# Optimization experiments

Measured on AMD Instinct MI355X. Metric: run time of the kernel, lower is better.

Reference implementation:

```python
import jax, jax.numpy as jnp
import numpy as np

T, B, E, H = 2048, 2, 1024, 16
DH = E // H  # head_dim = 64


def setup_inputs() -> dict:
    key = jax.random.key(0)
    ks = jax.random.split(key, 5)
    query = jax.random.normal(ks[0], (T, B, E), dtype=jnp.float32)
    # self-attention: key/value are passed but unused by the module
    k_in = query
    v_in = query
    # xavier-ish scaled params
    in_proj_weight = jax.random.normal(ks[1], (3 * E, E), dtype=jnp.float32) * (E ** -0.5)
    in_proj_bias = jnp.zeros((3 * E,), dtype=jnp.float32)
    out_w = jax.random.normal(ks[2], (E, E), dtype=jnp.float32) * (E ** -0.5)
    out_b = jnp.zeros((E,), dtype=jnp.float32)
    return {"query": query, "key": k_in, "value": v_in,
            "in_proj_weight": in_proj_weight, "in_proj_bias": in_proj_bias,
            "out_w": out_w, "out_b": out_b}


def reference(query, key, value, in_proj_weight, in_proj_bias, out_w, out_b):
    # query: [T, B, E] (fairseq Time x Batch x Channel)
    t, b, e = query.shape
    scaling = DH ** -0.5
    # fused QKV projection: in_proj_weight [3E, E]
    qkv = jnp.einsum('tbe,fe->tbf', query, in_proj_weight) + in_proj_bias  # [T,B,3E]
    q, k, v = jnp.split(qkv, 3, axis=-1)
    q = q * scaling
    # split heads -> [T, B, H, DH]
    q = q.reshape(t, b, H, DH)
    k = k.reshape(t, b, H, DH)
    v = v.reshape(t, b, H, DH)
    # attention scores [B, H, T, T]
    scores = jnp.einsum('tbhd,sbhd->bhts', q, k)
    probs = jax.nn.softmax(scores, axis=-1)
    # weighted sum -> [T, B, H, DH] -> [T, B, E]
    attn = jnp.einsum('bhts,sbhd->tbhd', probs, v).reshape(t, b, e)
    # output projection (LinearSuper with sample dims == super dims)
    out = jnp.einsum('tbe,oe->tbo', attn, out_w) + out_b
    return out
```

## Files before the change

### kernel.cpp

```cpp
#include <hip/hip_runtime.h>
#include <hip/hip_bf16.h>
#include <stdint.h>

#define T_DIM 2048
#define B_DIM 2
#define E_DIM 1024
#define H_DIM 16
#define DH    64
#define MROWS (T_DIM * B_DIM)
#define QKVN  (3 * E_DIM)

typedef __attribute__((ext_vector_type(8))) __bf16 bf16x8;
typedef __attribute__((ext_vector_type(4))) float f32x4;
typedef __attribute__((ext_vector_type(4))) uint32_t u32x4;

typedef __attribute__((address_space(1))) const uint32_t gu32;
typedef __attribute__((address_space(3))) uint32_t lu32;

#define GLL(gp, lp) __builtin_amdgcn_global_load_lds((gu32*)(gp), (lu32*)(lp), 16, 0, 0)

static __device__ __forceinline__ unsigned short f2bf(float f) {
    uint32_t u = __float_as_uint(f);
    u += 0x7FFFu + ((u >> 16) & 1u);
    return (unsigned short)(u >> 16);
}

__global__ void k_cvt(const float* __restrict__ in, unsigned short* __restrict__ out, int n) {
    int i = (blockIdx.x * 256 + threadIdx.x) * 8;
    if (i >= n) return;
    float4 a = *(const float4*)(in + i);
    float4 b = *(const float4*)(in + i + 4);
    union { unsigned short s[8]; u32x4 v; } r;
    r.s[0] = f2bf(a.x); r.s[1] = f2bf(a.y); r.s[2] = f2bf(a.z); r.s[3] = f2bf(a.w);
    r.s[4] = f2bf(b.x); r.s[5] = f2bf(b.y); r.s[6] = f2bf(b.z); r.s[7] = f2bf(b.w);
    *(u32x4*)(out + i) = r.v;
}

template <int STORE_BF16, int SCALE_Q>
__global__ __launch_bounds__(256) void k_gemm_bt(
    const unsigned short* __restrict__ A,
    const unsigned short* __restrict__ B,
    const float* __restrict__ bias,
    void* __restrict__ C,
    int M, int N, int K)
{
    __shared__ unsigned short As[128 * 64];
    __shared__ unsigned short Bs[128 * 64];
    const int tid = threadIdx.x;
    const int wid = tid >> 6, lane = tid & 63;
    const int m0 = blockIdx.y * 128, n0 = blockIdx.x * 128;

    const unsigned short* ag[4];
    const unsigned short* bg[4];
    unsigned lo[4];
#pragma unroll
    for (int j = 0; j < 4; ++j) {
        int o = (wid * 4 + j) * 1024 + lane * 16;
        int r = o >> 7;
        int c = (o >> 4) & 7;
        int cs = (c ^ (r & 7)) * 8;
        ag[j] = A + (long)(m0 + r) * K + cs;
        bg[j] = B + (long)(n0 + r) * K + cs;
        lo[j] = (unsigned)((wid * 4 + j) * 1024);
    }

    f32x4 acc[4][4] = {};
    const int wr = wid >> 1, wc = wid & 1;
    const int nk = K >> 6;

    for (int kt = 0; kt < nk; ++kt) {
#pragma unroll
        for (int j = 0; j < 4; ++j) {
            GLL(ag[j], (char*)As + lo[j]);
            GLL(bg[j], (char*)Bs + lo[j]);
            ag[j] += 64;
            bg[j] += 64;
        }
        __syncthreads();

        bf16x8 af[4][2], bfr[4][2];
#pragma unroll
        for (int i = 0; i < 4; ++i) {
            int ra = wr * 64 + i * 16 + (lane & 15);
            int rb = wc * 64 + i * 16 + (lane & 15);
#pragma unroll
            for (int kk = 0; kk < 2; ++kk) {
                int sa = ((kk * 4 + (lane >> 4)) ^ (ra & 7)) * 16;
                int sb = ((kk * 4 + (lane >> 4)) ^ (rb & 7)) * 16;
                af[i][kk]  = *(const bf16x8*)((char*)As + ra * 128 + sa);
                bfr[i][kk] = *(const bf16x8*)((char*)Bs + rb * 128 + sb);
            }
        }
#pragma unroll
        for (int kk = 0; kk < 2; ++kk)
#pragma unroll
            for (int mi = 0; mi < 4; ++mi)
#pragma unroll
                for (int ni = 0; ni < 4; ++ni)
                    acc[mi][ni] = __builtin_amdgcn_mfma_f32_16x16x32_bf16(
                        af[mi][kk], bfr[ni][kk], acc[mi][ni], 0, 0, 0);
        __syncthreads();
    }

#pragma unroll
    for (int mi = 0; mi < 4; ++mi)
#pragma unroll
        for (int ni = 0; ni < 4; ++ni) {
            int col = n0 + wc * 64 + ni * 16 + (lane & 15);
            float bv = bias[col];
            float scl = (SCALE_Q && col < 1024) ? 0.125f : 1.0f;
#pragma unroll
            for (int r = 0; r < 4; ++r) {
                int row = m0 + wr * 64 + mi * 16 + (lane >> 4) * 4 + r;
                float v = (acc[mi][ni][r] + bv) * scl;
                if (STORE_BF16)
                    ((unsigned short*)C)[(long)row * N + col] = f2bf(v);
                else
                    ((float*)C)[(long)row * N + col] = v;
            }
        }
}

__global__ __launch_bounds__(256) void k_transpose_v(
    const unsigned short* __restrict__ qkv, unsigned short* __restrict__ Vt)
{
    __shared__ unsigned short tile[64 * 64];
    const int bh = blockIdx.x >> 5, tt = blockIdx.x & 31;
    const int b = bh >> 4, h = bh & 15;
    const int tid = threadIdx.x;

    {
        int tr = tid >> 3;
        int s0 = tid & 7;
#pragma unroll
        for (int rr = 0; rr < 2; ++rr) {
            int t = tr + rr * 32;
            u32x4 v = *(const u32x4*)(qkv + ((long)(tt * 64 + t) * 2 + b) * 3072 + 2048 + h * 64 + s0 * 8);
            int slot = s0 ^ (t & 7) ^ ((t >> 3) & 7);
            *(u32x4*)((char*)tile + t * 128 + slot * 16) = v;
        }
    }
    __syncthreads();
    {
        int d = tid >> 3;
        int t8 = (tid & 7) * 8;
#pragma unroll
        for (int rr = 0; rr < 2; ++rr) {
            int dd = d + rr * 32;
            union { unsigned short s[8]; u32x4 v; } r;
#pragma unroll
            for (int i = 0; i < 8; ++i) {
                int t = t8 + i;
                int slot = (dd >> 3) ^ (t & 7) ^ ((t >> 3) & 7);
                r.s[i] = *(const unsigned short*)((char*)tile + t * 128 + slot * 16 + (dd & 7) * 2);
            }
            *(u32x4*)(Vt + ((long)bh * 64 + dd) * 2048 + tt * 64 + t8) = r.v;
        }
    }
}

__global__ __launch_bounds__(512) void k_attn(
    const unsigned short* __restrict__ qkv,
    const unsigned short* __restrict__ Vt,
    unsigned short* __restrict__ attn)
{
    __shared__ unsigned short Ks[2 * 64 * 64];
    __shared__ unsigned short Vs[2 * 64 * 64];
    __shared__ unsigned short Ps[8 * 16 * 64];
    const int tid = threadIdx.x, wid = tid >> 6, lane = tid & 63;
    const int bh = blockIdx.x >> 4, tq = blockIdx.x & 15;
    const int b = bh >> 4, h = bh & 15;

    bf16x8 qf[2];
#pragma unroll
    for (int kk = 0; kk < 2; ++kk) {
        int t = tq * 128 + wid * 16 + (lane & 15);
        qf[kk] = *(const bf16x8*)(qkv + (long)(t * 2 + b) * 3072 + h * 64 + kk * 32 + (lane >> 4) * 8);
    }

    const int srow = wid * 8 + (lane >> 3);
    const int cs = ((lane & 7) ^ (srow & 7)) * 8;
    const unsigned short* kg = qkv + (long)(srow * 2 + b) * 3072 + 1024 + h * 64 + cs;
    const unsigned short* vg = Vt + ((long)bh * 64 + srow) * 2048 + cs;
    const unsigned lo = wid * 1024;

    union { uint32_t u[4]; bf16x8 v; } onesu;
    onesu.u[0] = onesu.u[1] = onesu.u[2] = onesu.u[3] = 0x3F803F80u;
    const bf16x8 ones = onesu.v;

    f32x4 acc[4] = {};
    f32x4 suma = {};

    GLL(kg, (char*)Ks + lo);
    GLL(vg, (char*)Vs + lo);
    kg += 64 * 6144;
    vg += 64;

    for (int st = 0; st < 32; ++st) {
        const int cur = st & 1;
        if (st < 31) {
            GLL(kg, (char*)Ks + (cur ^ 1) * 8192 + lo);
            GLL(vg, (char*)Vs + (cur ^ 1) * 8192 + lo);
            kg += 64 * 6144;
            vg += 64;
            asm volatile("s_waitcnt vmcnt(2)" ::: "memory");
        } else {
            asm volatile("s_waitcnt vmcnt(0)" ::: "memory");
        }
        __builtin_amdgcn_s_barrier();

        const char* kbase = (const char*)Ks + cur * 8192;
        const char* vbase = (const char*)Vs + cur * 8192;

        bf16x8 kf[4][2];
#pragma unroll
        for (int ni = 0; ni < 4; ++ni) {
            int row = ni * 16 + (lane & 15);
#pragma unroll
            for (int kk = 0; kk < 2; ++kk) {
                int sl = ((kk * 4 + (lane >> 4)) ^ (row & 7)) * 16;
                kf[ni][kk] = *(const bf16x8*)(kbase + row * 128 + sl);
            }
        }
        f32x4 sc[4] = {};
#pragma unroll
        for (int kk = 0; kk < 2; ++kk)
#pragma unroll
            for (int ni = 0; ni < 4; ++ni)
                sc[ni] = __builtin_amdgcn_mfma_f32_16x16x32_bf16(
                    qf[kk], kf[ni][kk], sc[ni], 0, 0, 0);

#pragma unroll
        for (int ni = 0; ni < 4; ++ni)
#pragma unroll
            for (int r = 0; r < 4; ++r) {
                float p = __expf(sc[ni][r]);
                int q = (lane >> 4) * 4 + r;
                int scol = ni * 16 + (lane & 15);
                int off = wid * 2048 + q * 128 + ((scol * 2) ^ ((q & 7) << 4));
                *(unsigned short*)((char*)Ps + off) = f2bf(p);
            }

        bf16x8 pf[2], vf[4][2];
#pragma unroll
        for (int kk = 0; kk < 2; ++kk) {
            int q = lane & 15;
            int sl = ((kk * 4 + (lane >> 4)) ^ (q & 7)) * 16;
            pf[kk] = *(const bf16x8*)((char*)Ps + wid * 2048 + q * 128 + sl);
        }
#pragma unroll
        for (int nd = 0; nd < 4; ++nd) {
            int row = nd * 16 + (lane & 15);
#pragma unroll
            for (int kk = 0; kk < 2; ++kk) {
                int sl = ((kk * 4 + (lane >> 4)) ^ (row & 7)) * 16;
                vf[nd][kk] = *(const bf16x8*)(vbase + row * 128 + sl);
            }
        }
#pragma unroll
        for (int kk = 0; kk < 2; ++kk) {
            suma = __builtin_amdgcn_mfma_f32_16x16x32_bf16(pf[kk], ones, suma, 0, 0, 0);
#pragma unroll
            for (int nd = 0; nd < 4; ++nd)
                acc[nd] = __builtin_amdgcn_mfma_f32_16x16x32_bf16(
                    pf[kk], vf[nd][kk], acc[nd], 0, 0, 0);
        }
        __builtin_amdgcn_s_barrier();
    }

#pragma unroll
    for (int nd = 0; nd < 4; ++nd)
#pragma unroll
        for (int r = 0; r < 4; ++r) {
            int t = tq * 128 + wid * 16 + (lane >> 4) * 4 + r;
            int e = h * 64 + nd * 16 + (lane & 15);
            attn[(long)(t * 2 + b) * 1024 + e] = f2bf(acc[nd][r] / suma[r]);
        }
}

extern "C" void kernel_launch(void* const* d_in, const int* in_sizes, int n_in,
                              void* d_out, int out_size, void* d_ws, size_t ws_size,
                              hipStream_t stream) {
    const float* query = (const float*)d_in[0];
    const float* ipw   = (const float*)d_in[3];
    const float* ipb   = (const float*)d_in[4];
    const float* ow    = (const float*)d_in[5];
    const float* ob    = (const float*)d_in[6];
    float* out = (float*)d_out;

    char* ws = (char*)d_ws;
    unsigned short* Xb   = (unsigned short*)(ws);
    unsigned short* Wb   = (unsigned short*)(ws + (8l << 20));
    unsigned short* OWb  = (unsigned short*)(ws + (14l << 20));
    unsigned short* qkvp = (unsigned short*)(ws + (16l << 20));
    unsigned short* Vtp  = (unsigned short*)(ws + (40l << 20));
    unsigned short* attn = (unsigned short*)(ws + (48l << 20));

    k_cvt<<<2048, 256, 0, stream>>>(query, Xb, MROWS * E_DIM);
    k_cvt<<<1536, 256, 0, stream>>>(ipw, Wb, QKVN * E_DIM);
    k_cvt<<<512, 256, 0, stream>>>(ow, OWb, E_DIM * E_DIM);

    k_gemm_bt<1, 1><<<dim3(QKVN / 128, MROWS / 128), 256, 0, stream>>>(
        Xb, Wb, ipb, qkvp, MROWS, QKVN, E_DIM);

    k_transpose_v<<<1024, 256, 0, stream>>>(qkvp, Vtp);

    k_attn<<<512, 512, 0, stream>>>(qkvp, Vtp, attn);

    k_gemm_bt<0, 0><<<dim3(E_DIM / 128, MROWS / 128), 256, 0, stream>>>(
        attn, OWb, ob, out, MROWS, E_DIM, E_DIM);
}
```

Before: 235.7 us.

## Merge conversion kernels, use exp2 softmax, and give each attention wave two query tiles

The three fp32-to-bf16 conversion launches become one kernel. The query scale now folds in log2(e), so the softmax uses the hardware exp2 builtin instead of __expf. The attention kernel drops to 256 threads, each wave handling 32 query rows as two 16-row tiles, so every K/V fragment read from LDS feeds twice as many MFMAs; P is stored to LDS in packed 8-byte writes. The V transpose permutes the key order inside each 64-key block, and the P column layout is permuted the same way so the products still line up. The cost is higher register pressure per wave and fewer waves per block to hide latency.

```diff
diff --git a/kernel.cpp b/kernel.cpp
--- a/kernel.cpp
+++ b/kernel.cpp
@@ -1,6 +1,7 @@
 #include <hip/hip_runtime.h>
 #include <hip/hip_bf16.h>
 #include <stdint.h>
+#include <math.h>
 
 #define T_DIM 2048
 #define B_DIM 2
@@ -13,11 +14,20 @@
 typedef __attribute__((ext_vector_type(8))) __bf16 bf16x8;
 typedef __attribute__((ext_vector_type(4))) float f32x4;
 typedef __attribute__((ext_vector_type(4))) uint32_t u32x4;
+typedef __attribute__((ext_vector_type(2))) uint32_t u32x2;
 
 typedef __attribute__((address_space(1))) const uint32_t gu32;
 typedef __attribute__((address_space(3))) uint32_t lu32;
 
 #define GLL(gp, lp) __builtin_amdgcn_global_load_lds((gu32*)(gp), (lu32*)(lp), 16, 0, 0)
+
+#define QSCALE 0.18033688011112042f
+
+#if __has_builtin(__builtin_amdgcn_exp2f)
+#define EXP2(x) __builtin_amdgcn_exp2f(x)
+#else
+#define EXP2(x) exp2f(x)
+#endif
 
 static __device__ __forceinline__ unsigned short f2bf(float f) {
     uint32_t u = __float_as_uint(f);
@@ -25,15 +35,21 @@
     return (unsigned short)(u >> 16);
 }
 
-__global__ void k_cvt(const float* __restrict__ in, unsigned short* __restrict__ out, int n) {
-    int i = (blockIdx.x * 256 + threadIdx.x) * 8;
-    if (i >= n) return;
-    float4 a = *(const float4*)(in + i);
-    float4 b = *(const float4*)(in + i + 4);
+__global__ void k_cvt3(const float* __restrict__ q,  const float* __restrict__ w,
+                       const float* __restrict__ o,
+                       unsigned short* __restrict__ qo, unsigned short* __restrict__ wo,
+                       unsigned short* __restrict__ oo) {
+    long i = (long)(blockIdx.x * 256 + threadIdx.x) * 8;
+    const float* src; unsigned short* dst; long off;
+    if (i < 4194304)      { src = q; dst = qo; off = i; }
+    else if (i < 7340032) { src = w; dst = wo; off = i - 4194304; }
+    else                  { src = o; dst = oo; off = i - 7340032; }
+    float4 a = *(const float4*)(src + off);
+    float4 b = *(const float4*)(src + off + 4);
     union { unsigned short s[8]; u32x4 v; } r;
     r.s[0] = f2bf(a.x); r.s[1] = f2bf(a.y); r.s[2] = f2bf(a.z); r.s[3] = f2bf(a.w);
     r.s[4] = f2bf(b.x); r.s[5] = f2bf(b.y); r.s[6] = f2bf(b.z); r.s[7] = f2bf(b.w);
-    *(u32x4*)(out + i) = r.v;
+    *(u32x4*)(dst + off) = r.v;
 }
 
 template <int STORE_BF16, int SCALE_Q>
@@ -108,7 +124,7 @@
         for (int ni = 0; ni < 4; ++ni) {
             int col = n0 + wc * 64 + ni * 16 + (lane & 15);
             float bv = bias[col];
-            float scl = (SCALE_Q && col < 1024) ? 0.125f : 1.0f;
+            float scl = (SCALE_Q && col < 1024) ? QSCALE : 1.0f;
 #pragma unroll
             for (int r = 0; r < 4; ++r) {
                 int row = m0 + wr * 64 + mi * 16 + (lane >> 4) * 4 + r;
@@ -150,7 +166,8 @@
             union { unsigned short s[8]; u32x4 v; } r;
 #pragma unroll
             for (int i = 0; i < 8; ++i) {
-                int t = t8 + i;
+                int pos = t8 + i;
+                int t = (pos >> 2) + 16 * (pos & 3);
                 int slot = (dd >> 3) ^ (t & 7) ^ ((t >> 3) & 7);
                 r.s[i] = *(const unsigned short*)((char*)tile + t * 128 + slot * 16 + (dd & 7) * 2);
             }
@@ -159,51 +176,66 @@
     }
 }
 
-__global__ __launch_bounds__(512) void k_attn(
+__global__ __launch_bounds__(256, 2) void k_attn(
     const unsigned short* __restrict__ qkv,
     const unsigned short* __restrict__ Vt,
     unsigned short* __restrict__ attn)
 {
     __shared__ unsigned short Ks[2 * 64 * 64];
     __shared__ unsigned short Vs[2 * 64 * 64];
-    __shared__ unsigned short Ps[8 * 16 * 64];
+    __shared__ unsigned short Ps[4 * 32 * 64];
     const int tid = threadIdx.x, wid = tid >> 6, lane = tid & 63;
     const int bh = blockIdx.x >> 4, tq = blockIdx.x & 15;
     const int b = bh >> 4, h = bh & 15;
 
-    bf16x8 qf[2];
-#pragma unroll
-    for (int kk = 0; kk < 2; ++kk) {
-        int t = tq * 128 + wid * 16 + (lane & 15);
-        qf[kk] = *(const bf16x8*)(qkv + (long)(t * 2 + b) * 3072 + h * 64 + kk * 32 + (lane >> 4) * 8);
-    }
-
-    const int srow = wid * 8 + (lane >> 3);
-    const int cs = ((lane & 7) ^ (srow & 7)) * 8;
-    const unsigned short* kg = qkv + (long)(srow * 2 + b) * 3072 + 1024 + h * 64 + cs;
-    const unsigned short* vg = Vt + ((long)bh * 64 + srow) * 2048 + cs;
-    const unsigned lo = wid * 1024;
+    bf16x8 qf[2][2];
+#pragma unroll
+    for (int mi = 0; mi < 2; ++mi)
+#pragma unroll
+        for (int kk = 0; kk < 2; ++kk) {
+            int t = tq * 128 + wid * 32 + mi * 16 + (lane & 15);
+            qf[mi][kk] = *(const bf16x8*)(qkv + (long)(t * 2 + b) * 3072 + h * 64 + kk * 32 + (lane >> 4) * 8);
+        }
+
+    const unsigned short* kg[2];
+    const unsigned short* vg[2];
+    unsigned lo[2];
+#pragma unroll
+    for (int j = 0; j < 2; ++j) {
+        int o = (wid * 2 + j) * 1024 + lane * 16;
+        int r = o >> 7, c = (o >> 4) & 7;
+        int cs = (c ^ (r & 7)) * 8;
+        kg[j] = qkv + (long)(r * 2 + b) * 3072 + 1024 + h * 64 + cs;
+        vg[j] = Vt + ((long)bh * 64 + r) * 2048 + cs;
+        lo[j] = (unsigned)((wid * 2 + j) * 1024);
+    }
 
     union { uint32_t u[4]; bf16x8 v; } onesu;
     onesu.u[0] = onesu.u[1] = onesu.u[2] = onesu.u[3] = 0x3F803F80u;
     const bf16x8 ones = onesu.v;
 
-    f32x4 acc[4] = {};
-    f32x4 suma = {};
-
-    GLL(kg, (char*)Ks + lo);
-    GLL(vg, (char*)Vs + lo);
-    kg += 64 * 6144;
-    vg += 64;
+    f32x4 acc[2][4] = {};
+    f32x4 suma[2] = {};
+
+#pragma unroll
+    for (int j = 0; j < 2; ++j) {
+        GLL(kg[j], (char*)Ks + lo[j]);
+        GLL(vg[j], (char*)Vs + lo[j]);
+        kg[j] += 64 * 6144;
+        vg[j] += 64;
+    }
 
     for (int st = 0; st < 32; ++st) {
         const int cur = st & 1;
         if (st < 31) {
-            GLL(kg, (char*)Ks + (cur ^ 1) * 8192 + lo);
-            GLL(vg, (char*)Vs + (cur ^ 1) * 8192 + lo);
-            kg += 64 * 6144;
-            vg += 64;
-            asm volatile("s_waitcnt vmcnt(2)" ::: "memory");
+#pragma unroll
+            for (int j = 0; j < 2; ++j) {
+                GLL(kg[j], (char*)Ks + (cur ^ 1) * 8192 + lo[j]);
+                GLL(vg[j], (char*)Vs + (cur ^ 1) * 8192 + lo[j]);
+                kg[j] += 64 * 6144;
+                vg[j] += 64;
+            }
+            asm volatile("s_waitcnt vmcnt(4)" ::: "memory");
         } else {
             asm volatile("s_waitcnt vmcnt(0)" ::: "memory");
         }
@@ -222,32 +254,42 @@
                 kf[ni][kk] = *(const bf16x8*)(kbase + row * 128 + sl);
             }
         }
-        f32x4 sc[4] = {};
+        f32x4 sc[2][4] = {};
 #pragma unroll
         for (int kk = 0; kk < 2; ++kk)
 #pragma unroll
-            for (int ni = 0; ni < 4; ++ni)
-                sc[ni] = __builtin_amdgcn_mfma_f32_16x16x32_bf16(
-                    qf[kk], kf[ni][kk], sc[ni], 0, 0, 0);
-
-#pragma unroll
-        for (int ni = 0; ni < 4; ++ni)
+            for (int mi = 0; mi < 2; ++mi)
+#pragma unroll
+                for (int ni = 0; ni < 4; ++ni)
+                    sc[mi][ni] = __builtin_amdgcn_mfma_f32_16x16x32_bf16(
+                        qf[mi][kk], kf[ni][kk], sc[mi][ni], 0, 0, 0);
+
+        const int c = lane & 15;
+#pragma unroll
+        for (int mi = 0; mi < 2; ++mi)
 #pragma unroll
             for (int r = 0; r < 4; ++r) {
-                float p = __expf(sc[ni][r]);
-                int q = (lane >> 4) * 4 + r;
-                int scol = ni * 16 + (lane & 15);
-                int off = wid * 2048 + q * 128 + ((scol * 2) ^ ((q & 7) << 4));
-                *(unsigned short*)((char*)Ps + off) = f2bf(p);
-            }
-
-        bf16x8 pf[2], vf[4][2];
-#pragma unroll
-        for (int kk = 0; kk < 2; ++kk) {
-            int q = lane & 15;
-            int sl = ((kk * 4 + (lane >> 4)) ^ (q & 7)) * 16;
-            pf[kk] = *(const bf16x8*)((char*)Ps + wid * 2048 + q * 128 + sl);
-        }
+                float e0 = EXP2(sc[mi][0][r]);
+                float e1 = EXP2(sc[mi][1][r]);
+                float e2 = EXP2(sc[mi][2][r]);
+                float e3 = EXP2(sc[mi][3][r]);
+                int q = mi * 16 + (lane >> 4) * 4 + r;
+                u32x2 w;
+                w.x = (uint32_t)f2bf(e0) | ((uint32_t)f2bf(e1) << 16);
+                w.y = (uint32_t)f2bf(e2) | ((uint32_t)f2bf(e3) << 16);
+                int off = wid * 4096 + q * 128 + (((c >> 1) ^ (q & 7)) << 4) + (c & 1) * 8;
+                *(u32x2*)((char*)Ps + off) = w;
+            }
+
+        bf16x8 pf[2][2], vf[4][2];
+#pragma unroll
+        for (int mi = 0; mi < 2; ++mi)
+#pragma unroll
+            for (int kk = 0; kk < 2; ++kk) {
+                int q = mi * 16 + (lane & 15);
+                int sl = ((kk * 4 + (lane >> 4)) ^ (q & 7)) * 16;
+                pf[mi][kk] = *(const bf16x8*)((char*)Ps + wid * 4096 + q * 128 + sl);
+            }
 #pragma unroll
         for (int nd = 0; nd < 4; ++nd) {
             int row = nd * 16 + (lane & 15);
@@ -258,24 +300,29 @@
             }
         }
 #pragma unroll
-        for (int kk = 0; kk < 2; ++kk) {
-            suma = __builtin_amdgcn_mfma_f32_16x16x32_bf16(pf[kk], ones, suma, 0, 0, 0);
-#pragma unroll
-            for (int nd = 0; nd < 4; ++nd)
-                acc[nd] = __builtin_amdgcn_mfma_f32_16x16x32_bf16(
-                    pf[kk], vf[nd][kk], acc[nd], 0, 0, 0);
-        }
+        for (int kk = 0; kk < 2; ++kk)
+#pragma unroll
+            for (int mi = 0; mi < 2; ++mi) {
+                suma[mi] = __builtin_amdgcn_mfma_f32_16x16x32_bf16(
+                    pf[mi][kk], ones, suma[mi], 0, 0, 0);
+#pragma unroll
+                for (int nd = 0; nd < 4; ++nd)
+                    acc[mi][nd] = __builtin_amdgcn_mfma_f32_16x16x32_bf16(
+                        pf[mi][kk], vf[nd][kk], acc[mi][nd], 0, 0, 0);
+            }
         __builtin_amdgcn_s_barrier();
     }
 
 #pragma unroll
-    for (int nd = 0; nd < 4; ++nd)
-#pragma unroll
-        for (int r = 0; r < 4; ++r) {
-            int t = tq * 128 + wid * 16 + (lane >> 4) * 4 + r;
-            int e = h * 64 + nd * 16 + (lane & 15);
-            attn[(long)(t * 2 + b) * 1024 + e] = f2bf(acc[nd][r] / suma[r]);
-        }
+    for (int mi = 0; mi < 2; ++mi)
+#pragma unroll
+        for (int nd = 0; nd < 4; ++nd)
+#pragma unroll
+            for (int r = 0; r < 4; ++r) {
+                int t = tq * 128 + wid * 32 + mi * 16 + (lane >> 4) * 4 + r;
+                int e = h * 64 + nd * 16 + (lane & 15);
+                attn[(long)(t * 2 + b) * 1024 + e] = f2bf(acc[mi][nd][r] / suma[mi][r]);
+            }
 }
 
 extern "C" void kernel_launch(void* const* d_in, const int* in_sizes, int n_in,
@@ -296,16 +343,14 @@
     unsigned short* Vtp  = (unsigned short*)(ws + (40l << 20));
     unsigned short* attn = (unsigned short*)(ws + (48l << 20));
 
-    k_cvt<<<2048, 256, 0, stream>>>(query, Xb, MROWS * E_DIM);
-    k_cvt<<<1536, 256, 0, stream>>>(ipw, Wb, QKVN * E_DIM);
-    k_cvt<<<512, 256, 0, stream>>>(ow, OWb, E_DIM * E_DIM);
+    k_cvt3<<<4096, 256, 0, stream>>>(query, ipw, ow, Xb, Wb, OWb);
 
     k_gemm_bt<1, 1><<<dim3(QKVN / 128, MROWS / 128), 256, 0, stream>>>(
         Xb, Wb, ipb, qkvp, MROWS, QKVN, E_DIM);
 
     k_transpose_v<<<1024, 256, 0, stream>>>(qkvp, Vtp);
 
-    k_attn<<<512, 512, 0, stream>>>(qkvp, Vtp, attn);
+    k_attn<<<512, 256, 0, stream>>>(qkvp, Vtp, attn);
 
     k_gemm_bt<0, 0><<<dim3(E_DIM / 128, MROWS / 128), 256, 0, stream>>>(
         attn, OWb, ob, out, MROWS, E_DIM, E_DIM);
```

New measurement: 225.4 us. 1.05x faster.
